# Optimization experiments

Hardware: AMD Instinct MI355X
Metric: run time of the kernel (lower is better)

Reference implementation:

```python
import math
import jax, jax.numpy as jnp
import numpy as np

TWO_PI = 2.0 * math.pi
BETA = 1.0
K_COUP = 1.0
A_ANC = 0.08
OMEGA_ANC = TWO_PI * 200.0
B, P, N = 64, 256, 4096


def setup_inputs() -> dict:
    key = jax.random.key(0)
    k1, k2, k3 = jax.random.split(key, 3)
    t = jax.random.uniform(k1, (1,), dtype=jnp.float32)
    phi = jax.random.uniform(k2, (B, N), dtype=jnp.float32) * TWO_PI
    xi = jax.random.uniform(k3, (P, N), dtype=jnp.float32) * TWO_PI
    return {"t": t, "phi": phi, "xi": xi}


def reference(t, phi, xi):
    # diff: (B, P, N)
    diff = phi[:, None, :] - xi[None, :, :]
    m = jnp.cos(diff).sum(-1)                      # (B, P)
    weights = jax.nn.softmax(BETA * m / N, axis=-1)  # (B, P)
    coupling = jnp.einsum('bp,bpn->bn', weights, jnp.sin(diff))  # (B, N)
    dphi = K_COUP * coupling + A_ANC * jnp.sin(OMEGA_ANC * t - phi)
    return dphi
```

## Files before the change

### kernel.cpp

```cpp
#include <hip/hip_runtime.h>
#include <hip/hip_fp16.h>
#include <math.h>

#define B_SZ 64
#define P_SZ 256
#define N_SZ 4096
#define NC2 32
#define A_ANC 0.08f
#define OMEGA_ANC 1256.6370614359172f

typedef _Float16 h2v __attribute__((ext_vector_type(2)));

__device__ __forceinline__ float fdot2f(__half2 a, __half2 b, float c) {
#if __has_builtin(__builtin_amdgcn_fdot2)
    return __builtin_amdgcn_fdot2(__builtin_bit_cast(h2v, a),
                                  __builtin_bit_cast(h2v, b), c, false);
#else
    float2 af = __half22float2(a), bf = __half22float2(b);
    return fmaf(af.x, bf.x, fmaf(af.y, bf.y, c));
#endif
}

__global__ __launch_bounds__(256) void k_trig(const float* __restrict__ phi,
                                              const float* __restrict__ xi,
                                              __half2* __restrict__ XP,
                                              __half2* __restrict__ PPt) {
    int idx = blockIdx.x * 256 + threadIdx.x;
    const int PN = P_SZ * N_SZ;
    if (idx < PN) {
        float s, c;
        __sincosf(xi[idx], &s, &c);
        XP[idx] = __floats2half2_rn(c, s);
    } else {
        int j = idx - PN;
        float s, c;
        __sincosf(phi[j], &s, &c);
        int b = j >> 12;
        int n = j & (N_SZ - 1);
        PPt[n * B_SZ + b] = __floats2half2_rn(c, s);
    }
}

__global__ __launch_bounds__(256) void k_mpart(const __half2* __restrict__ XP,
                                               const __half2* __restrict__ PPt,
                                               float* __restrict__ m_part) {
    const int pt = blockIdx.x;
    const int nc = blockIdx.y;
    const int tid = threadIdx.x;
    const int b = tid & 63;
    const int g = tid >> 6;

    __shared__ __half2 xs[128][20];
    __shared__ float red[4][64][17];

    const int p0 = pt * 16, n0 = nc * 128;
    for (int idx = tid; idx < 16 * 128; idx += 256) {
        int p_l = idx >> 7, n_l = idx & 127;
        xs[n_l][p_l] = XP[(p0 + p_l) * N_SZ + n0 + n_l];
    }
    __syncthreads();

    float acc[16];
#pragma unroll
    for (int j = 0; j < 16; ++j) acc[j] = 0.f;

    for (int i = 0; i < 32; ++i) {
        int n_l = 4 * i + g;
        __half2 pp = PPt[(n0 + n_l) * B_SZ + b];
        const __half2* row = &xs[n_l][0];
#pragma unroll
        for (int j = 0; j < 16; ++j)
            acc[j] = fdot2f(row[j], pp, acc[j]);
    }

#pragma unroll
    for (int j = 0; j < 16; ++j) red[g][b][j] = acc[j];
    __syncthreads();
    if (tid < 64) {
#pragma unroll
        for (int j = 0; j < 16; ++j) {
            float s = red[0][tid][j] + red[1][tid][j] + red[2][tid][j] + red[3][tid][j];
            m_part[(nc * 64 + tid) * 256 + p0 + j] = s;
        }
    }
}

__global__ __launch_bounds__(256) void k_weights(const float* __restrict__ m_part,
                                                 float* __restrict__ weights) {
    const int b = blockIdx.x;
    const int tid = threadIdx.x;
    const int wv = tid >> 6;
    __shared__ float sred[8];

    float msum = 0.f;
#pragma unroll 8
    for (int c = 0; c < NC2; ++c)
        msum += m_part[(c * 64 + b) * 256 + tid];
    float logit = msum * (1.0f / 4096.0f);

    float v = logit;
    for (int o = 32; o > 0; o >>= 1) v = fmaxf(v, __shfl_xor(v, o));
    if ((tid & 63) == 0) sred[wv] = v;
    __syncthreads();
    float mx = fmaxf(fmaxf(sred[0], sred[1]), fmaxf(sred[2], sred[3]));
    float e = __expf(logit - mx);
    v = e;
    for (int o = 32; o > 0; o >>= 1) v += __shfl_xor(v, o);
    if ((tid & 63) == 0) sred[4 + wv] = v;
    __syncthreads();
    float s = sred[4] + sred[5] + sred[6] + sred[7];
    weights[b * 256 + tid] = e / s;
}

__global__ __launch_bounds__(256) void k_coupling(const __half2* __restrict__ XP,
                                                  const float* __restrict__ weights,
                                                  const float* __restrict__ phi,
                                                  const float* __restrict__ t_ptr,
                                                  float* __restrict__ out) {
    const int bt = blockIdx.x;
    const int nc = blockIdx.y;
    const int tid = threadIdx.x;
    const int b_l = tid >> 6;
    const int lane = tid & 63;

    __shared__ float wsh[4][256];
    for (int idx = tid; idx < 4 * 256; idx += 256) {
        int bb = idx >> 8, p = idx & 255;
        wsh[bb][p] = weights[(bt * 4 + bb) * 256 + p];
    }
    __syncthreads();

    const int n = nc * 64 + lane;
    const __half2* col = XP + n;
    float aC = 0.f, aS = 0.f;
#pragma unroll 8
    for (int p = 0; p < 256; ++p) {
        float2 cs = __half22float2(col[p * N_SZ]);
        float w = wsh[b_l][p];
        aC = fmaf(w, cs.x, aC);
        aS = fmaf(w, cs.y, aS);
    }

    const int b = bt * 4 + b_l;
    float ph = phi[b * N_SZ + n];
    float s, c;
    sincosf(ph, &s, &c);
    float wt = OMEGA_ANC * t_ptr[0];
    out[b * N_SZ + n] = fmaf(A_ANC, sinf(wt - ph), s * aC - c * aS);
}

extern "C" void kernel_launch(void* const* d_in, const int* in_sizes, int n_in,
                              void* d_out, int out_size, void* d_ws, size_t ws_size,
                              hipStream_t stream) {
    const float* t   = (const float*)d_in[0];
    const float* phi = (const float*)d_in[1];
    const float* xi  = (const float*)d_in[2];
    float* out = (float*)d_out;

    char* w = (char*)d_ws;
    __half2* XP  = (__half2*)w;
    __half2* PPt = (__half2*)(w + (size_t)P_SZ * N_SZ * 4);
    float* m_part = (float*)(w + 5u * 1024 * 1024);
    float* weights = (float*)(w + 13u * 1024 * 1024);

    k_trig<<<5120, 256, 0, stream>>>(phi, xi, XP, PPt);
    k_mpart<<<dim3(16, NC2), 256, 0, stream>>>(XP, PPt, m_part);
    k_weights<<<64, 256, 0, stream>>>(m_part, weights);
    k_coupling<<<dim3(16, 64), 256, 0, stream>>>(XP, weights, phi, t, out);
}
```

Before: 92.48 us.

## Fuse trig precompute into m-partial kernel and vectorize coupling loads

Removes the separate trig kernel. The m-partial kernel now computes cos/sin of xi on the fly, storing the half2 values to shared memory and to global for later use. It also recomputes the phi trig slice per block into shared memory instead of reading a transposed global buffer. The coupling kernel handles two columns per thread with 64-bit loads, float4 weight reads and float2 output stores, halving its grid. The cost is that phi sincos work is repeated across the 16 p-tiles, plus higher LDS usage and fewer coupling blocks.

```diff
diff --git a/kernel.cpp b/kernel.cpp
--- a/kernel.cpp
+++ b/kernel.cpp
@@ -21,29 +21,10 @@
 #endif
 }
 
-__global__ __launch_bounds__(256) void k_trig(const float* __restrict__ phi,
-                                              const float* __restrict__ xi,
-                                              __half2* __restrict__ XP,
-                                              __half2* __restrict__ PPt) {
-    int idx = blockIdx.x * 256 + threadIdx.x;
-    const int PN = P_SZ * N_SZ;
-    if (idx < PN) {
-        float s, c;
-        __sincosf(xi[idx], &s, &c);
-        XP[idx] = __floats2half2_rn(c, s);
-    } else {
-        int j = idx - PN;
-        float s, c;
-        __sincosf(phi[j], &s, &c);
-        int b = j >> 12;
-        int n = j & (N_SZ - 1);
-        PPt[n * B_SZ + b] = __floats2half2_rn(c, s);
-    }
-}
-
-__global__ __launch_bounds__(256) void k_mpart(const __half2* __restrict__ XP,
-                                               const __half2* __restrict__ PPt,
-                                               float* __restrict__ m_part) {
+__global__ __launch_bounds__(256, 2) void k_mpart_fused(const float* __restrict__ phi,
+                                                        const float* __restrict__ xi,
+                                                        __half2* __restrict__ XPg,
+                                                        float* __restrict__ m_part) {
     const int pt = blockIdx.x;
     const int nc = blockIdx.y;
     const int tid = threadIdx.x;
@@ -51,12 +32,24 @@
     const int g = tid >> 6;
 
     __shared__ __half2 xs[128][20];
+    __shared__ __half2 ps[128][66];
     __shared__ float red[4][64][17];
 
     const int p0 = pt * 16, n0 = nc * 128;
+
     for (int idx = tid; idx < 16 * 128; idx += 256) {
         int p_l = idx >> 7, n_l = idx & 127;
-        xs[n_l][p_l] = XP[(p0 + p_l) * N_SZ + n0 + n_l];
+        float s, c;
+        __sincosf(xi[(p0 + p_l) * N_SZ + n0 + n_l], &s, &c);
+        __half2 h = __floats2half2_rn(c, s);
+        xs[n_l][p_l] = h;
+        XPg[(p0 + p_l) * N_SZ + n0 + n_l] = h;
+    }
+    for (int idx = tid; idx < 64 * 128; idx += 256) {
+        int bb = idx >> 7, n_l = idx & 127;
+        float s, c;
+        __sincosf(phi[bb * N_SZ + n0 + n_l], &s, &c);
+        ps[n_l][bb] = __floats2half2_rn(c, s);
     }
     __syncthreads();
 
@@ -66,7 +59,7 @@
 
     for (int i = 0; i < 32; ++i) {
         int n_l = 4 * i + g;
-        __half2 pp = PPt[(n0 + n_l) * B_SZ + b];
+        __half2 pp = ps[n_l][b];
         const __half2* row = &xs[n_l][0];
 #pragma unroll
         for (int j = 0; j < 16; ++j)
@@ -112,11 +105,11 @@
     weights[b * 256 + tid] = e / s;
 }
 
-__global__ __launch_bounds__(256) void k_coupling(const __half2* __restrict__ XP,
-                                                  const float* __restrict__ weights,
-                                                  const float* __restrict__ phi,
-                                                  const float* __restrict__ t_ptr,
-                                                  float* __restrict__ out) {
+__global__ __launch_bounds__(256, 2) void k_coupling(const __half2* __restrict__ XP,
+                                                     const float* __restrict__ weights,
+                                                     const float* __restrict__ phi,
+                                                     const float* __restrict__ t_ptr,
+                                                     float* __restrict__ out) {
     const int bt = blockIdx.x;
     const int nc = blockIdx.y;
     const int tid = threadIdx.x;
@@ -130,23 +123,36 @@
     }
     __syncthreads();
 
-    const int n = nc * 64 + lane;
+    const int n = nc * 128 + 2 * lane;
     const __half2* col = XP + n;
-    float aC = 0.f, aS = 0.f;
-#pragma unroll 8
-    for (int p = 0; p < 256; ++p) {
-        float2 cs = __half22float2(col[p * N_SZ]);
-        float w = wsh[b_l][p];
-        aC = fmaf(w, cs.x, aC);
-        aS = fmaf(w, cs.y, aS);
+    float aC0 = 0.f, aS0 = 0.f, aC1 = 0.f, aS1 = 0.f;
+
+#pragma unroll 2
+    for (int p = 0; p < 256; p += 4) {
+        float4 w4 = *(const float4*)&wsh[b_l][p];
+        const float w[4] = {w4.x, w4.y, w4.z, w4.w};
+#pragma unroll
+        for (int k = 0; k < 4; ++k) {
+            uint2 v = *(const uint2*)&col[(p + k) * N_SZ];
+            __half2 h0 = __builtin_bit_cast(__half2, v.x);
+            __half2 h1 = __builtin_bit_cast(__half2, v.y);
+            aC0 = fmaf(w[k], __low2float(h0), aC0);
+            aS0 = fmaf(w[k], __high2float(h0), aS0);
+            aC1 = fmaf(w[k], __low2float(h1), aC1);
+            aS1 = fmaf(w[k], __high2float(h1), aS1);
+        }
     }
 
     const int b = bt * 4 + b_l;
-    float ph = phi[b * N_SZ + n];
-    float s, c;
-    sincosf(ph, &s, &c);
-    float wt = OMEGA_ANC * t_ptr[0];
-    out[b * N_SZ + n] = fmaf(A_ANC, sinf(wt - ph), s * aC - c * aS);
+    const float wt = OMEGA_ANC * t_ptr[0];
+    float2 ph2 = *(const float2*)&phi[b * N_SZ + n];
+    float s0, c0, s1, c1;
+    sincosf(ph2.x, &s0, &c0);
+    sincosf(ph2.y, &s1, &c1);
+    float2 o;
+    o.x = fmaf(A_ANC, sinf(wt - ph2.x), s0 * aC0 - c0 * aS0);
+    o.y = fmaf(A_ANC, sinf(wt - ph2.y), s1 * aC1 - c1 * aS1);
+    *(float2*)&out[b * N_SZ + n] = o;
 }
 
 extern "C" void kernel_launch(void* const* d_in, const int* in_sizes, int n_in,
@@ -158,13 +164,11 @@
     float* out = (float*)d_out;
 
     char* w = (char*)d_ws;
-    __half2* XP  = (__half2*)w;
-    __half2* PPt = (__half2*)(w + (size_t)P_SZ * N_SZ * 4);
-    float* m_part = (float*)(w + 5u * 1024 * 1024);
-    float* weights = (float*)(w + 13u * 1024 * 1024);
+    __half2* XP    = (__half2*)w;
+    float* m_part  = (float*)(w + 4u * 1024 * 1024);
+    float* weights = (float*)(w + 6u * 1024 * 1024);
 
-    k_trig<<<5120, 256, 0, stream>>>(phi, xi, XP, PPt);
-    k_mpart<<<dim3(16, NC2), 256, 0, stream>>>(XP, PPt, m_part);
+    k_mpart_fused<<<dim3(16, NC2), 256, 0, stream>>>(phi, xi, XP, m_part);
     k_weights<<<64, 256, 0, stream>>>(m_part, weights);
-    k_coupling<<<dim3(16, 64), 256, 0, stream>>>(XP, weights, phi, t, out);
+    k_coupling<<<dim3(16, NC2), 256, 0, stream>>>(XP, weights, phi, t, out);
 }
```

After: 100.4 us. 1.09x slower.
